# Optimization experiments

Hardware: AMD Instinct MI355X
Metric: run time of the kernel (lower is better)

Reference implementation:

```python
import jax, jax.numpy as jnp
import numpy as np
from jax import lax

B, N_BASES, C_IN, C_OUT, K, HW = 32, 5, 128, 128, 3, 56

def setup_inputs() -> dict:
    key = jax.random.key(0)
    k1, k2, k3 = jax.random.split(key, 3)
    x = jax.random.normal(k1, (B, C_IN, HW, HW), dtype=jnp.float32)
    weights = jax.random.normal(k2, (N_BASES, C_OUT, C_IN, K, K), dtype=jnp.float32) * 0.05
    scales = jax.random.uniform(k3, (N_BASES,), dtype=jnp.float32)
    return {"x": x, "weights": weights, "scales": scales}

def _binarize(w):
    # per-base: sign(w) * mean(|w|) over the whole weight tensor of that base
    m = jnp.mean(jnp.abs(w), axis=(1, 2, 3, 4), keepdims=True)  # [N,1,1,1,1]
    return jnp.sign(w) * m

def reference(x, weights, scales):
    # torch pads with constant value 1 (not zero) once, then all bases share it
    xp = jnp.pad(x, ((0, 0), (0, 0), (1, 1), (1, 1)), constant_values=1.0)
    wq = _binarize(weights)                              # [N,O,I,K,K]
    wf = wq.reshape(N_BASES * C_OUT, C_IN, K, K)          # fuse bases into one conv
    out = lax.conv_general_dilated(
        xp, wf, window_strides=(1, 1), padding='VALID',
        dimension_numbers=('NCHW', 'OIHW', 'NCHW'))      # [B, N*O, H, W]
    out = out.reshape(B, N_BASES, C_OUT, HW, HW)
    return jnp.einsum('bnohw,n->bohw', out, scales)
```

## Files before the change

kernel.cpp:

```cpp
#include <hip/hip_runtime.h>
#include <stdint.h>

#define N_BASES 5
#define WELEM (128 * 128 * 3 * 3)

typedef __attribute__((ext_vector_type(4))) float f32x4;
typedef __attribute__((ext_vector_type(8))) short bf16x8;

__device__ __forceinline__ unsigned short f2bf(float v) {
  union { float f; uint32_t u; } un;
  un.f = v;
  uint32_t r = un.u + 0x7FFFu + ((un.u >> 16) & 1u);
  return (unsigned short)(r >> 16);
}

__global__ __launch_bounds__(256) void prep_fused(
    const float* __restrict__ x, const float* __restrict__ w,
    unsigned short* __restrict__ xp, float* __restrict__ csum_part) {
  int bi = blockIdx.x;
  if (bi >= 1856) {
    int id = bi - 1856;
    int n = id >> 6;
    int chunk = id & 63;
    const f32x4* wb = (const f32x4*)(w + (size_t)n * WELEM + chunk * 2304);
    float s = 0.f;
    for (int i = threadIdx.x; i < 576; i += 256) {
      f32x4 v = wb[i];
      s += fabsf(v.x) + fabsf(v.y) + fabsf(v.z) + fabsf(v.w);
    }
    #pragma unroll
    for (int off = 32; off > 0; off >>= 1) s += __shfl_down(s, off);
    __shared__ float red[4];
    if ((threadIdx.x & 63) == 0) red[threadIdx.x >> 6] = s;
    __syncthreads();
    if (threadIdx.x == 0) csum_part[id] = red[0] + red[1] + red[2] + red[3];
    return;
  }
  int b = bi / 58;
  int hp = bi - b * 58;
  unsigned short* dst = xp + ((size_t)b * 58 + hp) * 58 * 128;
  int gh = hp - 1;
  if ((unsigned)gh >= 56u) {
    uint4 ones = make_uint4(0x3F803F80u, 0x3F803F80u, 0x3F803F80u, 0x3F803F80u);
    for (int i = threadIdx.x; i < 928; i += 256) ((uint4*)dst)[i] = ones;
    return;
  }
  __shared__ unsigned short tile[128][61];
  const float* src = x + ((size_t)b * 128 * 56 + gh) * 56;
  for (int i = threadIdx.x; i < 128 * 14; i += 256) {
    int c = i / 14;
    int k = i - c * 14;
    f32x4 v = *(const f32x4*)(src + (size_t)c * 3136 + k * 4);
    tile[c][1 + 4 * k + 0] = f2bf(v.x);
    tile[c][1 + 4 * k + 1] = f2bf(v.y);
    tile[c][1 + 4 * k + 2] = f2bf(v.z);
    tile[c][1 + 4 * k + 3] = f2bf(v.w);
  }
  if (threadIdx.x < 128) {
    tile[threadIdx.x][0] = 0x3F80;
    tile[threadIdx.x][57] = 0x3F80;
  }
  __syncthreads();
  for (int i = threadIdx.x; i < 928; i += 256) {
    int wp = i >> 4;
    int c8 = i & 15;
    union { uint4 q; unsigned short h[8]; } u;
    #pragma unroll
    for (int j = 0; j < 8; ++j) u.h[j] = tile[c8 * 8 + j][wp];
    *(uint4*)(dst + (size_t)wp * 128 + c8 * 8) = u.q;
  }
}

__global__ __launch_bounds__(256) void binweight_kernel(
    const float* __restrict__ w, const float* __restrict__ csum_part,
    const float* __restrict__ scales, unsigned short* __restrict__ wq) {
  __shared__ float parts[320];
  __shared__ float coef[N_BASES];
  for (int i = threadIdx.x; i < 320; i += 256) parts[i] = csum_part[i];
  __syncthreads();
  if (threadIdx.x < N_BASES) {
    float s = 0.f;
    #pragma unroll 8
    for (int k = 0; k < 64; ++k) s += parts[threadIdx.x * 64 + k];
    coef[threadIdx.x] = scales[threadIdx.x] * s * (1.0f / (float)WELEM);
  }
  __syncthreads();
  int f = blockIdx.x * 256 + threadIdx.x;
  float s = 0.f;
  #pragma unroll
  for (int n = 0; n < N_BASES; ++n) {
    float cn = coef[n];
    float v = w[n * WELEM + f];
    s += (v > 0.f) ? cn : ((v < 0.f) ? -cn : 0.f);
  }
  int o = f / 1152;
  int rem = f - o * 1152;
  int i = rem / 9;
  int t = rem - i * 9;
  int kb = i >> 5;
  int quad = (i >> 3) & 3;
  int e = i & 7;
  wq[((size_t)((t * 4 + kb) * 4 + quad) * 128 + o) * 8 + e] = f2bf(s);
}

__global__ __launch_bounds__(256, 3) void conv_kernel(
    const unsigned short* __restrict__ xp, const unsigned short* __restrict__ wq,
    float* __restrict__ out) {
  __shared__ unsigned short patch[23040];

  const int tid = threadIdx.x;
  const int blk = blockIdx.x;
  const int b = blk & 31;
  const int tile = blk >> 5;
  const int hi = tile >> 2;
  const int wi = tile & 3;
  const int h0 = hi * 8;
  const int w0 = (wi == 3) ? 40 : wi * 16;

  const size_t rowstride = 58 * 128;
  for (int i = tid; i < 2880; i += 256) {
    int sp = i >> 4;
    int c16 = i & 15;
    int ph = sp / 18;
    int pw = sp - ph * 18;
    const unsigned short* gp = xp + ((size_t)b * 58 + (h0 + ph)) * rowstride +
                               (size_t)(w0 + pw) * 128 + c16 * 8;
    uint4 v = *(const uint4*)gp;
    *(uint4*)&patch[sp * 128 + ((c16 ^ (sp & 7)) << 3)] = v;
  }
  __syncthreads();

  const int lane = tid & 63;
  const int wave = tid >> 6;
  const int mh = wave >> 1;
  const int nh = wave & 1;
  const int l15 = lane & 15;
  const int quad = lane >> 4;

  f32x4 acc[4][4];
  #pragma unroll
  for (int mf = 0; mf < 4; ++mf)
    #pragma unroll
    for (int nf = 0; nf < 4; ++nf) acc[mf][nf] = (f32x4)0.f;

  const unsigned short* wlane =
      wq + ((size_t)quad * 128 + nh * 64 + l15) * 8;

  #pragma unroll
  for (int t = 0; t < 9; ++t) {
    const int kh = t / 3;
    const int kw = t - kh * 3;
    int sp_mf[4];
    #pragma unroll
    for (int mf = 0; mf < 4; ++mf)
      sp_mf[mf] = (mh * 4 + mf + kh) * 18 + (l15 + kw);
    #pragma unroll
    for (int kb = 0; kb < 4; ++kb) {
      bf16x8 af[4], bfr[4];
      #pragma unroll
      for (int nf = 0; nf < 4; ++nf)
        bfr[nf] = *(const bf16x8*)(wlane + (size_t)(t * 4 + kb) * 4096 +
                                   nf * 128);
      #pragma unroll
      for (int mf = 0; mf < 4; ++mf) {
        int sp = sp_mf[mf];
        af[mf] = *(const bf16x8*)&patch[sp * 128 +
                                        (((kb * 4 + quad) ^ (sp & 7)) << 3)];
      }
      #pragma unroll
      for (int mf = 0; mf < 4; ++mf)
        #pragma unroll
        for (int nf = 0; nf < 4; ++nf)
          acc[mf][nf] = __builtin_amdgcn_mfma_f32_16x16x32_bf16(
              af[mf], bfr[nf], acc[mf][nf], 0, 0, 0);
    }
  }

  #pragma unroll
  for (int mf = 0; mf < 4; ++mf) {
    int h = h0 + mh * 4 + mf;
    #pragma unroll
    for (int nf = 0; nf < 4; ++nf) {
      int o = nh * 64 + nf * 16 + l15;
      float* p = out + (((size_t)b * 128 + o) * 56 + h) * 56 + w0 + quad * 4;
      *(f32x4*)p = acc[mf][nf];
    }
  }
}

extern "C" void kernel_launch(void* const* d_in, const int* in_sizes, int n_in,
                              void* d_out, int out_size, void* d_ws, size_t ws_size,
                              hipStream_t stream) {
  const float* x = (const float*)d_in[0];
  const float* w = (const float*)d_in[1];
  const float* scales = (const float*)d_in[2];
  float* out = (float*)d_out;

  float* csum_part = (float*)d_ws;
  unsigned short* wq = (unsigned short*)((char*)d_ws + 4096);
  unsigned short* xpad = (unsigned short*)((char*)d_ws + 512 * 1024);

  prep_fused<<<1856 + 320, 256, 0, stream>>>(x, w, xpad, csum_part);
  binweight_kernel<<<576, 256, 0, stream>>>(w, csum_part, scales, wq);
  conv_kernel<<<56 * 16, 256, 0, stream>>>(xpad, wq, out);
}
```

Before: 180.5 us.

## Double-buffer weight fragment loads across K-steps in conv kernel

The weight-fragment global loads are now software-pipelined with two register buffers. The first step's weights are prefetched before the patch staging and barrier, and each step's load is issued while the previous step's MFMAs run. The fully unrolled 36-step loop becomes a non-unrolled loop over pairs of steps, and A fragments are loaded one at a time inside the inner loop. This should hide global/L2 latency on the B operands, at the cost of one redundant load at the end, extra loop overhead and possibly different register pressure against the occupancy hint of 3.

```diff
diff --git a/kernel.cpp b/kernel.cpp
--- a/kernel.cpp
+++ b/kernel.cpp
@@ -117,6 +117,21 @@
   const int h0 = hi * 8;
   const int w0 = (wi == 3) ? 40 : wi * 16;
 
+  const int lane = tid & 63;
+  const int wave = tid >> 6;
+  const int mh = wave >> 1;
+  const int nh = wave & 1;
+  const int l15 = lane & 15;
+  const int quad = lane >> 4;
+
+  const unsigned short* wlane =
+      wq + ((size_t)quad * 128 + nh * 64 + l15) * 8;
+
+  bf16x8 b0[4], b1[4];
+  #pragma unroll
+  for (int nf = 0; nf < 4; ++nf)
+    b0[nf] = *(const bf16x8*)(wlane + nf * 128);
+
   const size_t rowstride = 58 * 128;
   for (int i = tid; i < 2880; i += 256) {
     int sp = i >> 4;
@@ -130,50 +145,41 @@
   }
   __syncthreads();
 
-  const int lane = tid & 63;
-  const int wave = tid >> 6;
-  const int mh = wave >> 1;
-  const int nh = wave & 1;
-  const int l15 = lane & 15;
-  const int quad = lane >> 4;
-
   f32x4 acc[4][4];
   #pragma unroll
   for (int mf = 0; mf < 4; ++mf)
     #pragma unroll
     for (int nf = 0; nf < 4; ++nf) acc[mf][nf] = (f32x4)0.f;
 
-  const unsigned short* wlane =
-      wq + ((size_t)quad * 128 + nh * 64 + l15) * 8;
-
-  #pragma unroll
-  for (int t = 0; t < 9; ++t) {
-    const int kh = t / 3;
-    const int kw = t - kh * 3;
-    int sp_mf[4];
-    #pragma unroll
-    for (int mf = 0; mf < 4; ++mf)
-      sp_mf[mf] = (mh * 4 + mf + kh) * 18 + (l15 + kw);
-    #pragma unroll
-    for (int kb = 0; kb < 4; ++kb) {
-      bf16x8 af[4], bfr[4];
+  auto compute = [&](int s, bf16x8 (&br)[4]) {
+    const int t = s >> 2;
+    const int kb = s & 3;
+    const int kh = (t * 11) >> 5;
+    const int kw = t - 3 * kh;
+    #pragma unroll
+    for (int mf = 0; mf < 4; ++mf) {
+      const int sp = (mh * 4 + mf + kh) * 18 + l15 + kw;
+      bf16x8 af = *(const bf16x8*)&patch[sp * 128 +
+                                         (((kb * 4 + quad) ^ (sp & 7)) << 3)];
       #pragma unroll
       for (int nf = 0; nf < 4; ++nf)
-        bfr[nf] = *(const bf16x8*)(wlane + (size_t)(t * 4 + kb) * 4096 +
-                                   nf * 128);
-      #pragma unroll
-      for (int mf = 0; mf < 4; ++mf) {
-        int sp = sp_mf[mf];
-        af[mf] = *(const bf16x8*)&patch[sp * 128 +
-                                        (((kb * 4 + quad) ^ (sp & 7)) << 3)];
-      }
-      #pragma unroll
-      for (int mf = 0; mf < 4; ++mf)
-        #pragma unroll
-        for (int nf = 0; nf < 4; ++nf)
-          acc[mf][nf] = __builtin_amdgcn_mfma_f32_16x16x32_bf16(
-              af[mf], bfr[nf], acc[mf][nf], 0, 0, 0);
+        acc[mf][nf] = __builtin_amdgcn_mfma_f32_16x16x32_bf16(
+            af, br[nf], acc[mf][nf], 0, 0, 0);
     }
+  };
+
+  #pragma unroll 1
+  for (int d = 0; d < 18; ++d) {
+    const int s = d * 2;
+    #pragma unroll
+    for (int nf = 0; nf < 4; ++nf)
+      b1[nf] = *(const bf16x8*)(wlane + (size_t)(s + 1) * 4096 + nf * 128);
+    compute(s, b0);
+    const int sn = (s + 2 < 36) ? s + 2 : 35;
+    #pragma unroll
+    for (int nf = 0; nf < 4; ++nf)
+      b0[nf] = *(const bf16x8*)(wlane + (size_t)sn * 4096 + nf * 128);
+    compute(s + 1, b1);
   }
 
   #pragma unroll
```

Result: faster. 154.1 us (-14.6%).
